# Kernel tuning notes

Hardware: AMD Instinct MI355X
Metric: run time of the kernel (lower is better)

## Reference

```python
import jax, jax.numpy as jnp
import numpy as np

N_NODES = 50000
IN_CH = 128
HIDDEN = 64
HEADS = 2
OUT_CH = 40
N_EDGES = 800000
NEG_SLOPE = 0.2


def gat_layer(x, src, dst, W, att_src, att_dst, bias, concat):
    # x: [N, F_in]; src/dst: [E] (self-loops already appended)
    N = x.shape[0]
    H, C = att_src.shape
    h = (x @ W).reshape(N, H, C)                      # [N, H, C]
    a_s = (h * att_src[None]).sum(-1)                 # [N, H]
    a_d = (h * att_dst[None]).sum(-1)                 # [N, H]
    e = jax.nn.leaky_relu(a_s[src] + a_d[dst], NEG_SLOPE)   # [E, H]
    # numerically-stable segment softmax over incoming edges per dst node
    m = jax.ops.segment_max(e, dst, num_segments=N)   # [N, H]
    m = jnp.where(jnp.isfinite(m), m, 0.0)
    m = jax.lax.stop_gradient(m)
    ex = jnp.exp(e - m[dst])                          # [E, H]
    denom = jax.ops.segment_sum(ex, dst, num_segments=N)    # [N, H]
    alpha = ex / (denom[dst] + 1e-16)                 # [E, H]
    out = jax.ops.segment_sum(alpha[:, :, None] * h[src], dst, num_segments=N)  # [N, H, C]
    out = out.reshape(N, H * C) if concat else out.mean(axis=1)
    return out + bias


def setup_inputs() -> dict:
    key = jax.random.key(0)
    ks = jax.random.split(key, 10)
    node_feat = jax.random.normal(ks[0], (N_NODES, IN_CH), dtype=jnp.float32)
    edge_index = jax.random.randint(ks[1], (2, N_EDGES), 0, N_NODES, dtype=jnp.int64)
    s1 = 1.0 / np.sqrt(IN_CH)
    s2 = 1.0 / np.sqrt(HIDDEN * HEADS)
    return {
        "node_feat": node_feat,
        "edge_index": edge_index,
        "W1": jax.random.normal(ks[2], (IN_CH, HEADS * HIDDEN), dtype=jnp.float32) * s1,
        "att_src1": jax.random.normal(ks[3], (HEADS, HIDDEN), dtype=jnp.float32) * s1,
        "att_dst1": jax.random.normal(ks[4], (HEADS, HIDDEN), dtype=jnp.float32) * s1,
        "b1": jnp.zeros((HEADS * HIDDEN,), dtype=jnp.float32),
        "W2": jax.random.normal(ks[5], (HEADS * HIDDEN, OUT_CH), dtype=jnp.float32) * s2,
        "att_src2": jax.random.normal(ks[6], (1, OUT_CH), dtype=jnp.float32) * s2,
        "att_dst2": jax.random.normal(ks[7], (1, OUT_CH), dtype=jnp.float32) * s2,
        "b2": jnp.zeros((OUT_CH,), dtype=jnp.float32),
    }


def reference(node_feat, edge_index, W1, att_src1, att_dst1, b1, W2, att_src2, att_dst2, b2):
    N = node_feat.shape[0]
    loop = jnp.arange(N, dtype=edge_index.dtype)
    src = jnp.concatenate([edge_index[0], loop])  # add self loops (PyG default)
    dst = jnp.concatenate([edge_index[1], loop])
    # eval mode: dropout is identity; use_bn=False
    x = gat_layer(node_feat, src, dst, W1, att_src1, att_dst1, b1, concat=True)
    x = jax.nn.elu(x)
    x = gat_layer(x, src, dst, W2, att_src2, att_dst2, b2, concat=False)
    return x
```

## Files before the change

### kernel.cpp

```cpp
#include <hip/hip_runtime.h>
#include <hip/hip_bf16.h>

#define N_NODES 50000
#define E0      800000
#define E_TOT   850000
#define G1_BLOCKS 782

typedef short short8 __attribute__((ext_vector_type(8)));
typedef float floatx4 __attribute__((ext_vector_type(4)));

__device__ __forceinline__ float lrelu(float x) { return x > 0.f ? x : 0.2f * x; }

__device__ __forceinline__ unsigned short f2bf(float f) {
    unsigned int u = __float_as_uint(f);
    u += 0x7fffu + ((u >> 16) & 1u);
    return (unsigned short)(u >> 16);
}
__device__ __forceinline__ float lo_bf(unsigned int p) { return __uint_as_float(p << 16); }
__device__ __forceinline__ float hi_bf(unsigned int p) { return __uint_as_float(p & 0xffff0000u); }

__device__ __forceinline__ short8 pack_bf16x8(float4 a, float4 b) {
    short8 r;
    r[0] = (short)f2bf(a.x); r[1] = (short)f2bf(a.y); r[2] = (short)f2bf(a.z); r[3] = (short)f2bf(a.w);
    r[4] = (short)f2bf(b.x); r[5] = (short)f2bf(b.y); r[6] = (short)f2bf(b.z); r[7] = (short)f2bf(b.w);
    return r;
}

__device__ __forceinline__ void fma8(float2* A, float w, uint4 h) {
    A[0].x += w * lo_bf(h.x); A[0].y += w * hi_bf(h.x);
    A[1].x += w * lo_bf(h.y); A[1].y += w * hi_bf(h.y);
    A[2].x += w * lo_bf(h.z); A[2].y += w * hi_bf(h.z);
    A[3].x += w * lo_bf(h.w); A[3].y += w * hi_bf(h.w);
}

__global__ __launch_bounds__(256) void hist_w(const int* __restrict__ ei, int* __restrict__ ghist,
                                              const float* __restrict__ W1, const float* __restrict__ W2,
                                              unsigned short* __restrict__ Wt1, unsigned short* __restrict__ Wt2) {
    __shared__ int h[256];
    int b = blockIdx.x, t = threadIdx.x;
    h[t] = 0;
    int i = b * 256 + t;
    if (i < 128 * 128) {
        int nn = i >> 7, k = i & 127;
        Wt1[i] = f2bf(W1[k * 128 + nn]);
    } else if (i < 128 * 128 + 48 * 128) {
        int j = i - 128 * 128;
        int nn = j >> 7, k = j & 127;
        Wt2[j] = (nn < 40) ? f2bf(W2[k * 40 + nn]) : (unsigned short)0;
    }
    __syncthreads();
    int base = b * 3328;
    #pragma unroll
    for (int k = 0; k < 13; ++k) {
        int e = base + t + k * 256;
        if (e < E_TOT) {
            int dst = (e < E0) ? ei[E0 + e] : (e - E0);
            atomicAdd(&h[dst >> 8], 1);
        }
    }
    __syncthreads();
    ghist[t * 256 + b] = h[t];
}

__global__ __launch_bounds__(256) void scan_local(const int* __restrict__ src, int* __restrict__ dst,
                                                  int* __restrict__ bsum, int n) {
    __shared__ int wsum[4];
    int t = threadIdx.x, lane = t & 63, wid = t >> 6;
    int idx = blockIdx.x * 1024 + t * 4;
    int4 v = make_int4(0, 0, 0, 0);
    if (idx < n) v = *reinterpret_cast<const int4*>(src + idx);
    int tsum = v.x + v.y + v.z + v.w;
    int sc = tsum;
    #pragma unroll
    for (int s = 1; s < 64; s <<= 1) {
        int up = __shfl_up(sc, s);
        if (lane >= s) sc += up;
    }
    if (lane == 63) wsum[wid] = sc;
    __syncthreads();
    int woff = 0;
    for (int w = 0; w < wid; ++w) woff += wsum[w];
    int b0 = woff + (sc - tsum);
    if (idx < n) {
        int4 o;
        o.x = b0;
        o.y = b0 + v.x;
        o.z = b0 + v.x + v.y;
        o.w = b0 + v.x + v.y + v.z;
        *reinterpret_cast<int4*>(dst + idx) = o;
    }
    if (t == 255) bsum[blockIdx.x] = woff + sc;
}

__global__ __launch_bounds__(256) void scan_addoff(int* __restrict__ arr, const int* __restrict__ bsum,
                                                   int* __restrict__ total, int n, int nb) {
    __shared__ int add_sh;
    int t = threadIdx.x;
    if (t < 64) {
        int v = (t < nb) ? bsum[t] : 0;
        int sc = v;
        #pragma unroll
        for (int s = 1; s < 64; s <<= 1) {
            int up = __shfl_up(sc, s);
            if (t >= s) sc += up;
        }
        if (t == (int)blockIdx.x) add_sh = sc - v;
        if (blockIdx.x == 0 && t == nb - 1) total[0] = sc;
    }
    __syncthreads();
    int idx = blockIdx.x * 1024 + t * 4;
    if (idx < n) {
        int add = add_sh;
        int4 v4 = *reinterpret_cast<int4*>(arr + idx);
        v4.x += add; v4.y += add; v4.z += add; v4.w += add;
        *reinterpret_cast<int4*>(arr + idx) = v4;
    }
}

__device__ __forceinline__ void gemm1_body(int blk, const float* __restrict__ X, const unsigned short* __restrict__ Wt,
                                           const float* __restrict__ asw, const float* __restrict__ adw,
                                           unsigned short* __restrict__ h1b, float* __restrict__ a_s,
                                           float* __restrict__ a_d, int nRows) {
    int t = threadIdx.x, lane = t & 63, wave = t >> 6;
    int l15 = lane & 15, g = lane >> 4;
    int r0 = blk * 64;
    int row = r0 + wave * 16 + l15;
    bool rv = row < nRows;
    const float* xrow = X + (size_t)(rv ? row : 0) * 128;

    float asv[8], adv[8];
    #pragma unroll
    for (int nt = 0; nt < 8; ++nt) { asv[nt] = asw[nt * 16 + l15]; adv[nt] = adw[nt * 16 + l15]; }

    floatx4 acc[8];
    #pragma unroll
    for (int nt = 0; nt < 8; ++nt) acc[nt] = (floatx4){0.f, 0.f, 0.f, 0.f};

    #pragma unroll
    for (int ks = 0; ks < 4; ++ks) {
        float4 xa = *reinterpret_cast<const float4*>(xrow + ks * 32 + g * 8);
        float4 xb = *reinterpret_cast<const float4*>(xrow + ks * 32 + g * 8 + 4);
        short8 af = pack_bf16x8(xa, xb);
        #pragma unroll
        for (int nt = 0; nt < 8; ++nt) {
            short8 bf = *reinterpret_cast<const short8*>(Wt + (size_t)(nt * 16 + l15) * 128 + ks * 32 + g * 8);
            acc[nt] = __builtin_amdgcn_mfma_f32_16x16x32_bf16(af, bf, acc[nt], 0, 0, 0);
        }
    }

    #pragma unroll
    for (int i = 0; i < 4; ++i) {
        int gr = r0 + wave * 16 + g * 4 + i;
        float s0 = 0.f, d0 = 0.f, s1 = 0.f, d1 = 0.f;
        #pragma unroll
        for (int nt = 0; nt < 4; ++nt) { s0 += acc[nt][i] * asv[nt]; d0 += acc[nt][i] * adv[nt]; }
        #pragma unroll
        for (int nt = 4; nt < 8; ++nt) { s1 += acc[nt][i] * asv[nt]; d1 += acc[nt][i] * adv[nt]; }
        #pragma unroll
        for (int sh = 1; sh < 16; sh <<= 1) {
            s0 += __shfl_xor(s0, sh); d0 += __shfl_xor(d0, sh);
            s1 += __shfl_xor(s1, sh); d1 += __shfl_xor(d1, sh);
        }
        if (gr < nRows) {
            if (l15 == 0) {
                a_s[gr * 2] = s0;     a_d[gr * 2] = d0;
                a_s[gr * 2 + 1] = s1; a_d[gr * 2 + 1] = d1;
            }
            #pragma unroll
            for (int nt = 0; nt < 8; ++nt)
                h1b[(size_t)gr * 128 + nt * 16 + l15] = f2bf(acc[nt][i]);
        }
    }
}

__global__ __launch_bounds__(256) void gemm1_scatter(const float* __restrict__ X, const unsigned short* __restrict__ Wt,
                                                     const float* __restrict__ asw, const float* __restrict__ adw,
                                                     unsigned short* __restrict__ h1b, float* __restrict__ a_s,
                                                     float* __restrict__ a_d,
                                                     const int* __restrict__ ei, const int* __restrict__ gbase,
                                                     unsigned int* __restrict__ tmpk) {
    __shared__ int cur[256];
    if (blockIdx.x < G1_BLOCKS) {
        gemm1_body(blockIdx.x, X, Wt, asw, adw, h1b, a_s, a_d, N_NODES);
    } else {
        int b = blockIdx.x - G1_BLOCKS, t = threadIdx.x;
        cur[t] = gbase[t * 256 + b];
        __syncthreads();
        int base = b * 3328;
        #pragma unroll
        for (int k = 0; k < 13; ++k) {
            int e = base + t + k * 256;
            if (e < E_TOT) {
                int src, dst;
                if (e < E0) { src = ei[e]; dst = ei[E0 + e]; }
                else        { src = dst = e - E0; }
                int pos = atomicAdd(&cur[dst >> 8], 1);
                tmpk[pos] = ((unsigned)dst << 16) | (unsigned)src;
            }
        }
    }
}

__global__ __launch_bounds__(256) void sort_w(const unsigned int* __restrict__ tmpk,
                                              const int* __restrict__ gbase,
                                              const float* __restrict__ a_s, const float* __restrict__ a_d,
                                              unsigned int* __restrict__ keys, uint4* __restrict__ ew,
                                              int* __restrict__ offs) {
    __shared__ unsigned int skey[8192];
    __shared__ unsigned int sorted[8192];
    __shared__ int h2[256], binb[256], cur2[256];
    int q = blockIdx.x, t = threadIdx.x;
    int start = gbase[q * 256];
    int end   = gbase[(q + 1) * 256];
    int n = end - start;
    if (n > 8192) n = 8192;
    h2[t] = 0;
    __syncthreads();
    for (int i = t; i < n; i += 256) {
        unsigned int k = tmpk[start + i];
        skey[i] = k;
        atomicAdd(&h2[(k >> 16) & 255], 1);
    }
    __syncthreads();
    if (t < 64) {
        int carry = 0;
        #pragma unroll
        for (int ch = 0; ch < 4; ++ch) {
            int idx = ch * 64 + t;
            int v = h2[idx];
            int sc = v;
            #pragma unroll
            for (int s = 1; s < 64; s <<= 1) {
                int up = __shfl_up(sc, s);
                if (t >= s) sc += up;
            }
            binb[idx] = sc - v + carry;
            cur2[idx] = sc - v + carry;
            carry += __shfl(sc, 63);
        }
    }
    __syncthreads();
    for (int i = t; i < n; i += 256) {
        unsigned int k = skey[i];
        int pos = atomicAdd(&cur2[(k >> 16) & 255], 1);
        sorted[pos] = k;
    }
    __syncthreads();
    for (int i = t; i < n; i += 256) {
        unsigned int k = sorted[i];
        keys[start + i] = k;
        int src = k & 0xFFFF, dst = k >> 16;
        float2 av = *reinterpret_cast<const float2*>(&a_s[src * 2]);
        float2 dv = *reinterpret_cast<const float2*>(&a_d[dst * 2]);
        uint4 e;
        e.x = k;
        e.y = __float_as_uint(__expf(lrelu(av.x + dv.x)));
        e.z = __float_as_uint(__expf(lrelu(av.y + dv.y)));
        e.w = 0;
        ew[start + i] = e;
    }
    int idx = q * 256 + t;
    if (idx <= N_NODES) offs[idx] = start + binb[t];
}

__global__ __launch_bounds__(256) void gemm2_mfma(const unsigned short* __restrict__ X2b,
                                                  const unsigned short* __restrict__ Wt,
                                                  const float* __restrict__ asw, const float* __restrict__ adw,
                                                  unsigned short* __restrict__ h2b, float* __restrict__ a_s,
                                                  float* __restrict__ a_d, int nRows) {
    int t = threadIdx.x, lane = t & 63, wave = t >> 6;
    int l15 = lane & 15, g = lane >> 4;
    int r0 = blockIdx.x * 64;
    int row = r0 + wave * 16 + l15;
    bool rv = row < nRows;
    const unsigned short* xrow = X2b + (size_t)(rv ? row : 0) * 128;

    float asv[3], adv[3];
    #pragma unroll
    for (int nt = 0; nt < 3; ++nt) {
        int col = nt * 16 + l15;
        asv[nt] = (col < 40) ? asw[col] : 0.f;
        adv[nt] = (col < 40) ? adw[col] : 0.f;
    }

    floatx4 acc[3];
    #pragma unroll
    for (int nt = 0; nt < 3; ++nt) acc[nt] = (floatx4){0.f, 0.f, 0.f, 0.f};

    #pragma unroll
    for (int ks = 0; ks < 4; ++ks) {
        short8 af = *reinterpret_cast<const short8*>(xrow + ks * 32 + g * 8);
        #pragma unroll
        for (int nt = 0; nt < 3; ++nt) {
            short8 bf = *reinterpret_cast<const short8*>(Wt + (size_t)(nt * 16 + l15) * 128 + ks * 32 + g * 8);
            acc[nt] = __builtin_amdgcn_mfma_f32_16x16x32_bf16(af, bf, acc[nt], 0, 0, 0);
        }
    }

    #pragma unroll
    for (int i = 0; i < 4; ++i) {
        int gr = r0 + wave * 16 + g * 4 + i;
        float ps = 0.f, pd = 0.f;
        #pragma unroll
        for (int nt = 0; nt < 3; ++nt) { ps += acc[nt][i] * asv[nt]; pd += acc[nt][i] * adv[nt]; }
        #pragma unroll
        for (int sh = 1; sh < 16; sh <<= 1) { ps += __shfl_xor(ps, sh); pd += __shfl_xor(pd, sh); }
        if (gr < nRows) {
            if (l15 == 0) { a_s[gr] = ps; a_d[gr] = pd; }
            #pragma unroll
            for (int nt = 0; nt < 3; ++nt) {
                int col = nt * 16 + l15;
                if (col < 40) h2b[(size_t)gr * 40 + col] = f2bf(acc[nt][i]);
            }
        }
    }
}

__global__ __launch_bounds__(256) void aggregate1(const unsigned short* __restrict__ Hb,
                                                  const uint4* __restrict__ ew, const int* __restrict__ offs,
                                                  const float* __restrict__ bias,
                                                  unsigned short* __restrict__ X2b, int n) {
    int t = threadIdx.x, lane = t & 63, wid = t >> 6;
    int node = blockIdx.x * 4 + wid;
    if (node >= n) return;
    int c = lane & 15, q = lane >> 4, head = c >> 3;
    int beg = offs[node], deg = offs[node + 1] - beg;
    float den0 = 0.f, den1 = 0.f;
    float2 acc0[4], acc1[4];
    #pragma unroll
    for (int m = 0; m < 4; ++m) { acc0[m] = make_float2(0.f, 0.f); acc1[m] = make_float2(0.f, 0.f); }

    for (int base = 0; base < deg; base += 64) {
        int nslots = min(64, deg - base);
        int s_l = 0; float w0_l = 0.f, w1_l = 0.f;
        if (lane < nslots) {
            uint4 e = ew[beg + base + lane];
            s_l = (int)(e.x & 0xFFFFu);
            w0_l = __uint_as_float(e.y);
            w1_l = __uint_as_float(e.z);
        }
        den0 += w0_l; den1 += w1_l;
        for (int j = 0; j < nslots; j += 8) {
            int j0 = j + q, j1 = j + 4 + q;
            int   sa  = __shfl(s_l, j0);
            float wa0 = __shfl(w0_l, j0), wa1 = __shfl(w1_l, j0);
            int   sb  = __shfl(s_l, j1);
            float wb0 = __shfl(w0_l, j1), wb1 = __shfl(w1_l, j1);
            float wa = head ? wa1 : wa0;
            float wb = head ? wb1 : wb0;
            uint4 ha = *reinterpret_cast<const uint4*>(&Hb[(size_t)sa * 128 + c * 8]);
            uint4 hb = *reinterpret_cast<const uint4*>(&Hb[(size_t)sb * 128 + c * 8]);
            fma8(acc0, wa, ha);
            fma8(acc1, wb, hb);
        }
    }
    #pragma unroll
    for (int m = 0; m < 4; ++m) { acc0[m].x += acc1[m].x; acc0[m].y += acc1[m].y; }
    #pragma unroll
    for (int sh = 32; sh > 0; sh >>= 1) { den0 += __shfl_xor(den0, sh); den1 += __shfl_xor(den1, sh); }
    #pragma unroll
    for (int m = 0; m < 4; ++m) {
        acc0[m].x += __shfl_xor(acc0[m].x, 16); acc0[m].x += __shfl_xor(acc0[m].x, 32);
        acc0[m].y += __shfl_xor(acc0[m].y, 16); acc0[m].y += __shfl_xor(acc0[m].y, 32);
    }
    if (q == 0) {
        float den = (head ? den1 : den0) + 1e-16f;
        float dinv = 1.f / den;
        float4 b0 = *reinterpret_cast<const float4*>(&bias[c * 8]);
        float4 b1 = *reinterpret_cast<const float4*>(&bias[c * 8 + 4]);
        float va[8] = {acc0[0].x, acc0[0].y, acc0[1].x, acc0[1].y, acc0[2].x, acc0[2].y, acc0[3].x, acc0[3].y};
        float bb[8] = {b0.x, b0.y, b0.z, b0.w, b1.x, b1.y, b1.z, b1.w};
        float o[8];
        #pragma unroll
        for (int k = 0; k < 8; ++k) {
            float v = va[k] * dinv + bb[k];
            o[k] = v > 0.f ? v : (__expf(v) - 1.f);
        }
        uint4 pk;
        pk.x = (unsigned)f2bf(o[0]) | ((unsigned)f2bf(o[1]) << 16);
        pk.y = (unsigned)f2bf(o[2]) | ((unsigned)f2bf(o[3]) << 16);
        pk.z = (unsigned)f2bf(o[4]) | ((unsigned)f2bf(o[5]) << 16);
        pk.w = (unsigned)f2bf(o[6]) | ((unsigned)f2bf(o[7]) << 16);
        *reinterpret_cast<uint4*>(&X2b[(size_t)node * 128 + c * 8]) = pk;
    }
}

__global__ __launch_bounds__(256) void aggregate2(const unsigned short* __restrict__ Hb,
                                                  const float* __restrict__ a_s, const float* __restrict__ a_d,
                                                  const int* __restrict__ offs, const unsigned int* __restrict__ keys,
                                                  const float* __restrict__ bias, float* __restrict__ out, int n) {
    int t = threadIdx.x, lane = t & 63, wid = t >> 6;
    int node = blockIdx.x * 4 + wid;
    if (node >= n) return;
    int g = lane / 5, c = lane - g * 5;
    bool dead = (g >= 12);
    if (dead) { g = 0; c = 0; }
    int beg = offs[node], deg = offs[node + 1] - beg;
    float adv = a_d[node];
    float den = 0.f;
    float2 acc0[4], acc1[4];
    #pragma unroll
    for (int m = 0; m < 4; ++m) { acc0[m] = make_float2(0.f, 0.f); acc1[m] = make_float2(0.f, 0.f); }

    for (int base = 0; base < deg; base += 48) {
        int nslots = min(48, deg - base);
        int s_l = 0; float w_l = 0.f;
        if (lane < nslots) {
            s_l = (int)(keys[beg + base + lane] & 0xFFFFu);
            w_l = __expf(lrelu(a_s[s_l] + adv));
        }
        den += w_l;
        for (int j = 0; j < nslots; j += 24) {
            int j0 = j + g, j1 = j + 12 + g;
            int   sa = __shfl(s_l, j0); float wa = __shfl(w_l, j0);
            int   sb = __shfl(s_l, j1); float wb = __shfl(w_l, j1);
            uint4 ha = *reinterpret_cast<const uint4*>(&Hb[(size_t)sa * 40 + c * 8]);
            uint4 hb = *reinterpret_cast<const uint4*>(&Hb[(size_t)sb * 40 + c * 8]);
            fma8(acc0, wa, ha);
            fma8(acc1, wb, hb);
        }
    }
    #pragma unroll
    for (int m = 0; m < 4; ++m) { acc0[m].x += acc1[m].x; acc0[m].y += acc1[m].y; }
    if (lane >= 60) {
        #pragma unroll
        for (int m = 0; m < 4; ++m) acc0[m] = make_float2(0.f, 0.f);
    }
    #pragma unroll
    for (int sh = 32; sh > 0; sh >>= 1) den += __shfl_xor(den, sh);
    #pragma unroll
    for (int m = 0; m < 4; ++m) {
        float ax = acc0[m].x, ay = acc0[m].y;
        ax += __shfl(ax, lane + 30); ay += __shfl(ay, lane + 30);
        ax += __shfl(ax, lane + 15); ay += __shfl(ay, lane + 15);
        float ax5 = __shfl(ax, lane + 5),  ay5 = __shfl(ay, lane + 5);
        float ax10 = __shfl(ax, lane + 10), ay10 = __shfl(ay, lane + 10);
        acc0[m].x = ax + ax5 + ax10;
        acc0[m].y = ay + ay5 + ay10;
    }
    if (lane < 5) {
        float dinv = 1.f / (den + 1e-16f);
        float4 b0 = *reinterpret_cast<const float4*>(&bias[c * 8]);
        float4 b1 = *reinterpret_cast<const float4*>(&bias[c * 8 + 4]);
        float4 o0, o1;
        o0.x = acc0[0].x * dinv + b0.x; o0.y = acc0[0].y * dinv + b0.y;
        o0.z = acc0[1].x * dinv + b0.z; o0.w = acc0[1].y * dinv + b0.w;
        o1.x = acc0[2].x * dinv + b1.x; o1.y = acc0[2].y * dinv + b1.y;
        o1.z = acc0[3].x * dinv + b1.z; o1.w = acc0[3].y * dinv + b1.w;
        *reinterpret_cast<float4*>(&out[(size_t)node * 40 + c * 8])     = o0;
        *reinterpret_cast<float4*>(&out[(size_t)node * 40 + c * 8 + 4]) = o1;
    }
}

extern "C" void kernel_launch(void* const* d_in, const int* in_sizes, int n_in,
                              void* d_out, int out_size, void* d_ws, size_t ws_size,
                              hipStream_t stream) {
    (void)in_sizes; (void)n_in; (void)out_size; (void)ws_size;
    const float* x    = (const float*)d_in[0];
    const int*   ei   = (const int*)d_in[1];
    const float* W1   = (const float*)d_in[2];
    const float* as1w = (const float*)d_in[3];
    const float* ad1w = (const float*)d_in[4];
    const float* b1   = (const float*)d_in[5];
    const float* W2   = (const float*)d_in[6];
    const float* as2w = (const float*)d_in[7];
    const float* ad2w = (const float*)d_in[8];
    const float* b2   = (const float*)d_in[9];
    float* out = (float*)d_out;

    float* ws = (float*)d_ws;
    float* h1slot = ws; ws += (size_t)N_NODES * 128;
    float* x2slot = ws; ws += (size_t)N_NODES * 128;
    float* a_s1 = ws; ws += N_NODES * 2;
    float* a_d1 = ws; ws += N_NODES * 2;
    float* a_s2 = ws; ws += N_NODES;
    float* a_d2 = ws; ws += N_NODES;
    float* h2slot = ws; ws += (size_t)N_NODES * 40;
    int* offs  = (int*)ws;
    int* ghist = offs + 50432;
    int* gbase = ghist + 65536;
    int* bsum  = gbase + 65536;
    int* total = bsum + 64;
    unsigned int* tmpk = (unsigned int*)(total + 4);
    unsigned int* keys = tmpk + E_TOT;
    uint4* ew = (uint4*)(keys + E_TOT);
    unsigned short* Wt1 = (unsigned short*)(ew + E_TOT);
    unsigned short* Wt2 = Wt1 + 128 * 128;

    unsigned short* h1b = (unsigned short*)h1slot;
    unsigned short* x2b = (unsigned short*)x2slot;
    unsigned short* h2b = (unsigned short*)h2slot;

    hist_w<<<256, 256, 0, stream>>>(ei, ghist, W1, W2, Wt1, Wt2);
    scan_local<<<64, 256, 0, stream>>>(ghist, gbase, bsum, 65536);
    scan_addoff<<<64, 256, 0, stream>>>(gbase, bsum, total, 65536, 64);
    gemm1_scatter<<<G1_BLOCKS + 256, 256, 0, stream>>>(x, Wt1, as1w, ad1w, h1b, a_s1, a_d1, ei, gbase, tmpk);
    sort_w<<<196, 256, 0, stream>>>(tmpk, gbase, a_s1, a_d1, keys, ew, offs);
    aggregate1<<<(N_NODES + 3) / 4, 256, 0, stream>>>(h1b, ew, offs, b1, x2b, N_NODES);
    gemm2_mfma<<<(N_NODES + 63) / 64, 256, 0, stream>>>(x2b, Wt2, as2w, ad2w, h2b, a_s2, a_d2, N_NODES);
    aggregate2<<<(N_NODES + 3) / 4, 256, 0, stream>>>(h2b, a_s2, a_d2, offs, keys, b2, out, N_NODES);
}
```

Baseline: 124.3 us.

## Locally sort scatter keys in LDS before writing coalesced bucket runs

The scatter phase of the radix partition now stages each block's edge keys in shared memory, builds a local histogram and scan, and sorts the keys by top digit before writing them out. Each bucket's keys then land as one contiguous run in global memory instead of being scattered one at a time through shared-atomic positions. The global histogram is also trimmed to the 196 digits actually used, so the scan kernels process fewer entries. The cost is extra shared memory and several block-wide synchronisations, which lower occupancy for the scatter blocks that share the kernel with the GEMM blocks.

```diff
diff --git a/kernel.cpp b/kernel.cpp
--- a/kernel.cpp
+++ b/kernel.cpp
@@ -5,6 +5,8 @@
 #define E0      800000
 #define E_TOT   850000
 #define G1_BLOCKS 782
+#define NDIG 196
+#define GH_N (NDIG * 256)
 
 typedef short short8 __attribute__((ext_vector_type(8)));
 typedef float floatx4 __attribute__((ext_vector_type(4)));
@@ -59,7 +61,7 @@
         }
     }
     __syncthreads();
-    ghist[t * 256 + b] = h[t];
+    if (t < NDIG) ghist[t * 256 + b] = h[t];
 }
 
 __global__ __launch_bounds__(256) void scan_local(const int* __restrict__ src, int* __restrict__ dst,
@@ -179,24 +181,55 @@
                                                      float* __restrict__ a_d,
                                                      const int* __restrict__ ei, const int* __restrict__ gbase,
                                                      unsigned int* __restrict__ tmpk) {
-    __shared__ int cur[256];
+    __shared__ unsigned int ek[3328];
+    __shared__ unsigned int lsorted[3328];
+    __shared__ int lh[256], lbase[256], lcur[256];
     if (blockIdx.x < G1_BLOCKS) {
         gemm1_body(blockIdx.x, X, Wt, asw, adw, h1b, a_s, a_d, N_NODES);
     } else {
         int b = blockIdx.x - G1_BLOCKS, t = threadIdx.x;
-        cur[t] = gbase[t * 256 + b];
+        int base = b * 3328;
+        int n = min(3328, E_TOT - base);
+        lh[t] = 0;
         __syncthreads();
-        int base = b * 3328;
-        #pragma unroll
-        for (int k = 0; k < 13; ++k) {
-            int e = base + t + k * 256;
-            if (e < E_TOT) {
-                int src, dst;
-                if (e < E0) { src = ei[e]; dst = ei[E0 + e]; }
-                else        { src = dst = e - E0; }
-                int pos = atomicAdd(&cur[dst >> 8], 1);
-                tmpk[pos] = ((unsigned)dst << 16) | (unsigned)src;
+        for (int i = t; i < n; i += 256) {
+            int e = base + i;
+            int src, dst;
+            if (e < E0) { src = ei[e]; dst = ei[E0 + e]; }
+            else        { src = dst = e - E0; }
+            unsigned int k = ((unsigned)dst << 16) | (unsigned)src;
+            ek[i] = k;
+            atomicAdd(&lh[dst >> 8], 1);
+        }
+        __syncthreads();
+        if (t < 64) {
+            int carry = 0;
+            #pragma unroll
+            for (int ch = 0; ch < 4; ++ch) {
+                int idx = ch * 64 + t;
+                int v = lh[idx];
+                int sc = v;
+                #pragma unroll
+                for (int s = 1; s < 64; s <<= 1) {
+                    int up = __shfl_up(sc, s);
+                    if (t >= s) sc += up;
+                }
+                lbase[idx] = sc - v + carry;
+                lcur[idx]  = sc - v + carry;
+                carry += __shfl(sc, 63);
             }
+        }
+        __syncthreads();
+        for (int i = t; i < n; i += 256) {
+            unsigned int k = ek[i];
+            int pos = atomicAdd(&lcur[k >> 24], 1);
+            lsorted[pos] = k;
+        }
+        __syncthreads();
+        for (int i = t; i < n; i += 256) {
+            unsigned int k = lsorted[i];
+            int d = k >> 24;
+            tmpk[gbase[d * 256 + b] + (i - lbase[d])] = k;
         }
     }
 }
@@ -480,8 +513,8 @@
     int* ghist = offs + 50432;
     int* gbase = ghist + 65536;
     int* bsum  = gbase + 65536;
-    int* total = bsum + 64;
-    unsigned int* tmpk = (unsigned int*)(total + 4);
+    int* total = gbase + GH_N;
+    unsigned int* tmpk = (unsigned int*)(bsum + 64);
     unsigned int* keys = tmpk + E_TOT;
     uint4* ew = (uint4*)(keys + E_TOT);
     unsigned short* Wt1 = (unsigned short*)(ew + E_TOT);
@@ -491,11 +524,13 @@
     unsigned short* x2b = (unsigned short*)x2slot;
     unsigned short* h2b = (unsigned short*)h2slot;
 
+    const int NB = (GH_N + 1023) / 1024;
+
     hist_w<<<256, 256, 0, stream>>>(ei, ghist, W1, W2, Wt1, Wt2);
-    scan_local<<<64, 256, 0, stream>>>(ghist, gbase, bsum, 65536);
-    scan_addoff<<<64, 256, 0, stream>>>(gbase, bsum, total, 65536, 64);
+    scan_local<<<NB, 256, 0, stream>>>(ghist, gbase, bsum, GH_N);
+    scan_addoff<<<NB, 256, 0, stream>>>(gbase, bsum, total, GH_N, NB);
     gemm1_scatter<<<G1_BLOCKS + 256, 256, 0, stream>>>(x, Wt1, as1w, ad1w, h1b, a_s1, a_d1, ei, gbase, tmpk);
-    sort_w<<<196, 256, 0, stream>>>(tmpk, gbase, a_s1, a_d1, keys, ew, offs);
+    sort_w<<<NDIG, 256, 0, stream>>>(tmpk, gbase, a_s1, a_d1, keys, ew, offs);
     aggregate1<<<(N_NODES + 3) / 4, 256, 0, stream>>>(h1b, ew, offs, b1, x2b, N_NODES);
     gemm2_mfma<<<(N_NODES + 63) / 64, 256, 0, stream>>>(x2b, Wt2, as2w, ad2w, h2b, a_s2, a_d2, N_NODES);
     aggregate2<<<(N_NODES + 3) / 4, 256, 0, stream>>>(h2b, a_s2, a_d2, offs, keys, b2, out, N_NODES);
```

Result: slower. 126.8 us (+2.0%).
